# Performance work log

Measured on AMD Instinct MI355X. Metric: run time of the kernel, lower is better.

Reference implementation:

```python
import jax, jax.numpy as jnp
import numpy as np

B, T, C, H, N = 2, 2048, 2048, 32, 64
EPS_GN = 1e-5 * 8 ** 2  # eps * head_size_divisor^2


def _bf16(t):
    # kernel inputs are cast to bfloat16 in the original module
    return t.astype(jnp.bfloat16).astype(jnp.float32)


def _rwkv7_scan(r, k, v, w, a, b, s0):
    """Generalized delta-rule recurrence (fused_recurrent_rwkv7 semantics).
    r,k,v,w,a,b: [B,T,H,N]; s0: [B,H,N,N] with layout [key, value].
    S_t = diag(exp(w_t)) S + b_t (a_t^T S) + k_t v_t^T ; o_t = r_t^T S_t."""
    def step(S, ts):
        rt, kt, vt, wt, at, bt = ts  # each [B,H,N]
        sa = jnp.einsum('bhk,bhkv->bhv', at, S)
        S = S * jnp.exp(wt)[..., None] + bt[..., None] * sa[..., None, :] + kt[..., None] * vt[..., None, :]
        o = jnp.einsum('bhk,bhkv->bhv', rt, S)
        return S, o
    mv = lambda t: jnp.moveaxis(t, 1, 0)  # [B,T,H,N] -> [T,B,H,N]
    S, o = jax.lax.scan(step, s0, (mv(r), mv(k), mv(v), mv(w), mv(a), mv(b)))
    return jnp.moveaxis(o, 0, 1), S


def _forward(x, shift_state, wkv_state, v_first, x_r, x_w, x_k, x_v, x_a, x_g,
             w0, w1, w2, a0, a1, a2, v0, v1, v2, g1, g2, k_k, k_a, r_k,
             W_r, W_k, W_v, W_o, ln_w, ln_b):
    xx = jnp.concatenate([shift_state[:, None, :], x[:, :-1]], axis=1) - x
    xr, xw, xk, xv, xa, xg = (x + xx * m for m in (x_r, x_w, x_k, x_v, x_a, x_g))
    r = xr @ W_r
    w = -jax.nn.softplus(-(w0 + jnp.tanh(xw @ w1) @ w2)) - 0.5
    k = xk @ W_k
    v = xv @ W_v
    v = v + (v_first - v) * jax.nn.sigmoid(v0 + (xv @ v1) @ v2)  # layer_id > 0 branch
    a = jax.nn.sigmoid(a0 + (xa @ a1) @ a2)
    g = jax.nn.sigmoid(xg @ g1) @ g2
    kk = (k * k_k).reshape(B, T, H, N)
    kk = kk / jnp.maximum(jnp.linalg.norm(kk, axis=-1, keepdims=True), 1e-12)
    kk = kk.reshape(B, T, C)
    k = k * (1.0 + (a - 1.0) * k_a)
    hd = lambda t: _bf16(t).reshape(B, T, H, N)
    o, S = _rwkv7_scan(hd(r), hd(k), hd(v), hd(w), hd(-kk), hd(kk * a), wkv_state)
    y = o.reshape(B, T, H, N)
    # GroupNorm with H groups over C channels
    mu = y.mean(-1, keepdims=True)
    var = ((y - mu) ** 2).mean(-1, keepdims=True)
    y = ((y - mu) / jnp.sqrt(var + EPS_GN)).reshape(B, T, C) * ln_w + ln_b
    rr, k4, vv = r.reshape(B, T, H, N), k.reshape(B, T, H, N), v.reshape(B, T, H, N)
    y = y + ((rr * k4 * r_k).sum(-1, keepdims=True) * vv).reshape(B, T, C)
    out = (y * g) @ W_o
    return out, x[:, -1], S


def setup_inputs() -> dict:
    key = jax.random.key(0)
    ks = iter(jax.random.split(key, 40))
    rn = lambda shape, s=0.02: jax.random.normal(next(ks), shape, jnp.float32) * s
    ru = lambda shape: jax.random.uniform(next(ks), shape, jnp.float32)
    return dict(
        x=rn((B, T, C), 1.0), shift_state=rn((B, C), 1.0),
        wkv_state=jnp.zeros((B, H, N, N), jnp.float32), v_first=rn((B, T, C), 1.0),
        x_r=ru((1, 1, C)), x_w=ru((1, 1, C)), x_k=ru((1, 1, C)),
        x_v=ru((1, 1, C)), x_a=ru((1, 1, C)), x_g=ru((1, 1, C)),
        w0=rn((1, 1, C), 0.5) - 4.0, w1=rn((C, 64)), w2=rn((64, C)),
        a0=jnp.zeros((1, 1, C), jnp.float32), a1=rn((C, 64)), a2=rn((64, C)),
        v0=jnp.ones((1, 1, C), jnp.float32), v1=rn((C, 32)), v2=rn((32, C)),
        g1=rn((C, 128)), g2=rn((128, C)),
        k_k=jnp.full((1, 1, C), 0.85, jnp.float32), k_a=jnp.ones((1, 1, C), jnp.float32),
        r_k=rn((H, N), 0.1),
        W_r=rn((C, C), C ** -0.5), W_k=rn((C, C), C ** -0.5),
        W_v=rn((C, C), C ** -0.5), W_o=rn((C, C), C ** -0.5),
        ln_w=jnp.ones((C,), jnp.float32), ln_b=jnp.zeros((C,), jnp.float32))


def reference(x, shift_state, wkv_state, v_first, x_r, x_w, x_k, x_v, x_a, x_g,
              w0, w1, w2, a0, a1, a2, v0, v1, v2, g1, g2, k_k, k_a, r_k,
              W_r, W_k, W_v, W_o, ln_w, ln_b):
    return _forward(x, shift_state, wkv_state, v_first, x_r, x_w, x_k, x_v, x_a, x_g,
                    w0, w1, w2, a0, a1, a2, v0, v1, v2, g1, g2, k_k, k_a, r_k,
                    W_r, W_k, W_v, W_o, ln_w, ln_b)
```

## Files before the change

### kernel.cpp

```cpp
#include <hip/hip_runtime.h>
#include <cstdint>
#include <cmath>

#define B_ 2
#define T_ 2048
#define C_ 2048
#define H_ 32
#define BT_ (B_ * T_)
#define BTC_ ((size_t)B_ * T_ * C_)
#define L_ 128
#define NC_ 16

typedef __attribute__((ext_vector_type(4))) float f32x4;
typedef __attribute__((ext_vector_type(2))) float f32x2;
typedef __attribute__((ext_vector_type(8))) short bf16x8;
typedef __attribute__((ext_vector_type(4))) unsigned short us4;
typedef __attribute__((ext_vector_type(4))) int i32x4;

__device__ __forceinline__ unsigned short f2bf(float f) {
  union { float f; unsigned int u; } c; c.f = f;
  unsigned int u = c.u;
  return (unsigned short)((u + 0x7FFFu + ((u >> 16) & 1u)) >> 16);
}
__device__ __forceinline__ float bf2f(unsigned short h) {
  union { unsigned int u; float f; } c; c.u = ((unsigned int)h) << 16;
  return c.f;
}
__device__ __forceinline__ float rlane(float v, int lane) {
  return __int_as_float(__builtin_amdgcn_readlane(__float_as_int(v), lane));
}
__device__ __forceinline__ void split4(f32x4 v, us4& h, us4& l) {
  h.x = f2bf(v.x); l.x = f2bf(v.x - bf2f(h.x));
  h.y = f2bf(v.y); l.y = f2bf(v.y - bf2f(h.y));
  h.z = f2bf(v.z); l.z = f2bf(v.z - bf2f(h.z));
  h.w = f2bf(v.w); l.w = f2bf(v.w - bf2f(h.w));
}
__device__ __forceinline__ void g2l(const void* g, void* l) {
  __builtin_amdgcn_global_load_lds((const __attribute__((address_space(1))) void*)g,
                                   (__attribute__((address_space(3))) void*)l, 16, 0, 0);
}

__global__ __launch_bounds__(256) void k_mix(
    const float* __restrict__ x, const float* __restrict__ shift,
    const float* __restrict__ m_r, const float* __restrict__ m_w,
    const float* __restrict__ m_k, const float* __restrict__ m_v,
    const float* __restrict__ m_a, const float* __restrict__ m_g,
    unsigned short* __restrict__ r_h, unsigned short* __restrict__ r_l,
    unsigned short* __restrict__ k_h, unsigned short* __restrict__ k_l,
    unsigned short* __restrict__ v_h, unsigned short* __restrict__ v_l,
    unsigned short* __restrict__ o_w, unsigned short* __restrict__ o_a,
    unsigned short* __restrict__ o_g,
    float* __restrict__ xlast) {
  size_t i4 = ((size_t)blockIdx.x * 256 + threadIdx.x) * 4;
  int c = (int)(i4 % C_);
  size_t bt = i4 / C_;
  int t = (int)(bt % T_);
  int b = (int)(bt / T_);
  f32x4 xv = *(const f32x4*)(x + i4);
  f32x4 pv = (t == 0) ? *(const f32x4*)(shift + (size_t)b * C_ + c)
                      : *(const f32x4*)(x + i4 - C_);
  f32x4 dx = pv - xv;
#define MIXHL(mp, oh, ol) { f32x4 mm = *(const f32x4*)(mp + c); f32x4 rr = xv + dx * mm; \
    us4 hh, ll; split4(rr, hh, ll); *(us4*)(oh + i4) = hh; *(us4*)(ol + i4) = ll; }
#define MIXH(mp, oh) { f32x4 mm = *(const f32x4*)(mp + c); f32x4 rr = xv + dx * mm; \
    us4 pk; pk.x = f2bf(rr.x); pk.y = f2bf(rr.y); pk.z = f2bf(rr.z); pk.w = f2bf(rr.w); \
    *(us4*)(oh + i4) = pk; }
  MIXHL(m_r, r_h, r_l) MIXHL(m_k, k_h, k_l) MIXHL(m_v, v_h, v_l)
  MIXH(m_w, o_w) MIXH(m_a, o_a) MIXH(m_g, o_g)
#undef MIXHL
#undef MIXH
  if (t == T_ - 1) *(f32x4*)(xlast + (size_t)b * C_ + c) = xv;
}

__global__ __launch_bounds__(256) void k_tr(const float* __restrict__ in,
                                            unsigned short* __restrict__ out,
                                            int R, int Cc) {
  __shared__ float tile[32][33];
  int c0 = blockIdx.x * 32, r0 = blockIdx.y * 32;
  int tid = threadIdx.x;
  int rr = tid >> 3, c4 = (tid & 7) * 4;
  f32x4 v = *(const f32x4*)(in + (size_t)(r0 + rr) * Cc + c0 + c4);
  tile[rr][c4] = v.x; tile[rr][c4 + 1] = v.y; tile[rr][c4 + 2] = v.z; tile[rr][c4 + 3] = v.w;
  __syncthreads();
  int cc = tid >> 3, r4 = (tid & 7) * 4;
  us4 o;
  o.x = f2bf(tile[r4][cc]); o.y = f2bf(tile[r4 + 1][cc]);
  o.z = f2bf(tile[r4 + 2][cc]); o.w = f2bf(tile[r4 + 3][cc]);
  *(us4*)(out + (size_t)(c0 + cc) * R + r0 + r4) = o;
}

__global__ __launch_bounds__(256) void k_trs(const float* __restrict__ in,
                                             unsigned short* __restrict__ oh,
                                             unsigned short* __restrict__ ol,
                                             int R, int Cc) {
  __shared__ float tile[32][33];
  int c0 = blockIdx.x * 32, r0 = blockIdx.y * 32;
  int tid = threadIdx.x;
  int rr = tid >> 3, c4 = (tid & 7) * 4;
  f32x4 v = *(const f32x4*)(in + (size_t)(r0 + rr) * Cc + c0 + c4);
  tile[rr][c4] = v.x; tile[rr][c4 + 1] = v.y; tile[rr][c4 + 2] = v.z; tile[rr][c4 + 3] = v.w;
  __syncthreads();
  int cc = tid >> 3, r4 = (tid & 7) * 4;
  f32x4 w = { tile[r4][cc], tile[r4 + 1][cc], tile[r4 + 2][cc], tile[r4 + 3][cc] };
  us4 h, l; split4(w, h, l);
  size_t o = (size_t)(c0 + cc) * R + r0 + r4;
  *(us4*)(oh + o) = h; *(us4*)(ol + o) = l;
}

__global__ __launch_bounds__(256) void k_gemm(
    const unsigned short* __restrict__ X, const unsigned short* __restrict__ Wt,
    void* __restrict__ out, int M, int N, int K, int mode) {
  __shared__ alignas(16) unsigned short As[128 * 32];
  __shared__ alignas(16) unsigned short Bs[128 * 32];
  const int tid = threadIdx.x;
  const int lane = tid & 63, wave = tid >> 6;
  const int wr = wave >> 1, wc = wave & 1;
  const int lm = lane & 15, lq = lane >> 4;
  const int gx = gridDim.x;
  const int nwg = gx * gridDim.y;
  const int bid = blockIdx.y * gx + blockIdx.x;
  const int sz = (bid & 7) * (nwg >> 3) + (bid >> 3);
  const int m0 = (sz / gx) * 128, n0 = (sz % gx) * 128;
  const int srow = (lane >> 2);
  const int kcol = (lane & 3) * 8;
  f32x4 acc[4][4];
#pragma unroll
  for (int i = 0; i < 4; ++i)
#pragma unroll
    for (int j = 0; j < 4; ++j) acc[i][j] = (f32x4){0.f, 0.f, 0.f, 0.f};

  for (int k0 = 0; k0 < K; k0 += 32) {
#pragma unroll
    for (int p = 0; p < 2; ++p) {
      int row = wave * 32 + p * 16 + srow;
      g2l(X + (size_t)(m0 + row) * K + k0 + kcol, As + (wave * 2 + p) * 512);
      int n = n0 + row; if (n > N - 1) n = N - 1;
      g2l(Wt + (size_t)n * K + k0 + kcol, Bs + (wave * 2 + p) * 512);
    }
    __syncthreads();
    bf16x8 af[4], bfr[4];
#pragma unroll
    for (int i = 0; i < 4; ++i)
      af[i] = *(const bf16x8*)(As + (size_t)(wr * 64 + i * 16 + lm) * 32 + lq * 8);
#pragma unroll
    for (int j = 0; j < 4; ++j)
      bfr[j] = *(const bf16x8*)(Bs + (size_t)(wc * 64 + j * 16 + lm) * 32 + lq * 8);
#pragma unroll
    for (int i = 0; i < 4; ++i)
#pragma unroll
      for (int j = 0; j < 4; ++j)
        acc[i][j] = __builtin_amdgcn_mfma_f32_16x16x32_bf16(af[i], bfr[j], acc[i][j], 0, 0, 0);
    __syncthreads();
  }
#pragma unroll
  for (int i = 0; i < 4; ++i)
#pragma unroll
    for (int j = 0; j < 4; ++j) {
      int n = n0 + wc * 64 + j * 16 + lm;
      if (n >= N) continue;
      int mb = m0 + wr * 64 + i * 16 + lq * 4;
#pragma unroll
      for (int r = 0; r < 4; ++r) {
        float val = acc[i][j][r];
        size_t off = (size_t)(mb + r) * N + n;
        if (mode == 0) {
          ((float*)out)[off] = val;
        } else {
          if (mode == 2) val = tanhf(val);
          else if (mode == 3) val = 1.0f / (1.0f + __expf(-val));
          ((unsigned short*)out)[off] = f2bf(val);
        }
      }
    }
}

__global__ __launch_bounds__(256) void k_gemm2(
    const unsigned short* __restrict__ Xh, const unsigned short* __restrict__ Xl, int xlo,
    const unsigned short* __restrict__ Wh, const unsigned short* __restrict__ Wl, int wlo,
    void* __restrict__ out, int M, int N, int K, int mode) {
  __shared__ alignas(16) unsigned short Ah[128 * 32];
  __shared__ alignas(16) unsigned short Al[128 * 32];
  __shared__ alignas(16) unsigned short Bh[128 * 32];
  __shared__ alignas(16) unsigned short Bl[128 * 32];
  const int tid = threadIdx.x;
  const int lane = tid & 63, wave = tid >> 6;
  const int wr = wave >> 1, wc = wave & 1;
  const int lm = lane & 15, lq = lane >> 4;
  const int gx = gridDim.x;
  const int nwg = gx * gridDim.y;
  const int bid = blockIdx.y * gx + blockIdx.x;
  const int sz = (bid & 7) * (nwg >> 3) + (bid >> 3);
  const int m0 = (sz / gx) * 128, n0 = (sz % gx) * 128;
  const int srow = (lane >> 2);
  const int kcol = (lane & 3) * 8;
  f32x4 acc[4][4];
#pragma unroll
  for (int i = 0; i < 4; ++i)
#pragma unroll
    for (int j = 0; j < 4; ++j) acc[i][j] = (f32x4){0.f, 0.f, 0.f, 0.f};

  for (int k0 = 0; k0 < K; k0 += 32) {
#pragma unroll
    for (int p = 0; p < 2; ++p) {
      int row = wave * 32 + p * 16 + srow;
      int off = (wave * 2 + p) * 512;
      size_t ga = (size_t)(m0 + row) * K + k0 + kcol;
      g2l(Xh + ga, Ah + off);
      if (xlo) g2l(Xl + ga, Al + off);
      int n = n0 + row; if (n > N - 1) n = N - 1;
      size_t gb = (size_t)n * K + k0 + kcol;
      g2l(Wh + gb, Bh + off);
      if (wlo) g2l(Wl + gb, Bl + off);
    }
    __syncthreads();
    bf16x8 ah[4], bh[4];
#pragma unroll
    for (int i = 0; i < 4; ++i)
      ah[i] = *(const bf16x8*)(Ah + (size_t)(wr * 64 + i * 16 + lm) * 32 + lq * 8);
#pragma unroll
    for (int j = 0; j < 4; ++j)
      bh[j] = *(const bf16x8*)(Bh + (size_t)(wc * 64 + j * 16 + lm) * 32 + lq * 8);
#pragma unroll
    for (int i = 0; i < 4; ++i)
#pragma unroll
      for (int j = 0; j < 4; ++j)
        acc[i][j] = __builtin_amdgcn_mfma_f32_16x16x32_bf16(ah[i], bh[j], acc[i][j], 0, 0, 0);
    if (xlo) {
      bf16x8 al[4];
#pragma unroll
      for (int i = 0; i < 4; ++i)
        al[i] = *(const bf16x8*)(Al + (size_t)(wr * 64 + i * 16 + lm) * 32 + lq * 8);
#pragma unroll
      for (int i = 0; i < 4; ++i)
#pragma unroll
        for (int j = 0; j < 4; ++j)
          acc[i][j] = __builtin_amdgcn_mfma_f32_16x16x32_bf16(al[i], bh[j], acc[i][j], 0, 0, 0);
    }
    if (wlo) {
      bf16x8 bl[4];
#pragma unroll
      for (int j = 0; j < 4; ++j)
        bl[j] = *(const bf16x8*)(Bl + (size_t)(wc * 64 + j * 16 + lm) * 32 + lq * 8);
#pragma unroll
      for (int i = 0; i < 4; ++i)
#pragma unroll
        for (int j = 0; j < 4; ++j)
          acc[i][j] = __builtin_amdgcn_mfma_f32_16x16x32_bf16(ah[i], bl[j], acc[i][j], 0, 0, 0);
    }
    __syncthreads();
  }
#pragma unroll
  for (int i = 0; i < 4; ++i)
#pragma unroll
    for (int j = 0; j < 4; ++j) {
      int n = n0 + wc * 64 + j * 16 + lm;
      if (n >= N) continue;
      int mb = m0 + wr * 64 + i * 16 + lq * 4;
#pragma unroll
      for (int r = 0; r < 4; ++r) {
        float val = acc[i][j][r];
        size_t off = (size_t)(mb + r) * N + n;
        if (mode == 0) {
          ((float*)out)[off] = val;
        } else {
          if (mode == 2) val = tanhf(val);
          else if (mode == 3) val = 1.0f / (1.0f + __expf(-val));
          ((unsigned short*)out)[off] = f2bf(val);
        }
      }
    }
}

__global__ __launch_bounds__(256) void k_pre(
    const float* __restrict__ rp, const float* __restrict__ kp, float* __restrict__ vp,
    const unsigned short* __restrict__ ww, const unsigned short* __restrict__ aa,
    const unsigned short* __restrict__ vv,
    const float* __restrict__ vfirst,
    const float* __restrict__ w0, const float* __restrict__ a0, const float* __restrict__ v0,
    const float* __restrict__ kkc, const float* __restrict__ kac,
    const float* __restrict__ rkw,
    unsigned short* __restrict__ rb, unsigned short* __restrict__ wb,
    unsigned short* __restrict__ kb, unsigned short* __restrict__ vb,
    unsigned short* __restrict__ ab, unsigned short* __restrict__ bb,
    float* __restrict__ dp) {
  int gw = blockIdx.x * 4 + (threadIdx.x >> 6);
  int l = threadIdx.x & 63;
  int h = gw & (H_ - 1);
  size_t bt = (size_t)(gw >> 5);
  size_t idx = bt * C_ + h * 64 + l;
  int c = h * 64 + l;
  float rf = rp[idx], kf = kp[idx], vr = vp[idx];
  float z = -(w0[c] + bf2f(ww[idx]));
  float sp = (z > 15.f) ? z : log1pf(__expf(z));
  float wv = -sp - 0.5f;
  float ag = 1.f / (1.f + __expf(-(a0[c] + bf2f(aa[idx]))));
  float sv = 1.f / (1.f + __expf(-(v0[c] + bf2f(vv[idx]))));
  float vf = vr + (vfirst[idx] - vr) * sv;
  float kkv = kf * kkc[c];
  float ss = kkv * kkv;
#pragma unroll
  for (int m = 1; m < 64; m <<= 1) ss += __shfl_xor(ss, m);
  float nrm = fmaxf(sqrtf(ss), 1e-12f);
  float kkn = kkv / nrm;
  float ks = kf * (1.f + (ag - 1.f) * kac[c]);
  vp[idx] = vf;
  float bon = rf * ks * rkw[c];
#pragma unroll
  for (int m = 1; m < 64; m <<= 1) bon += __shfl_xor(bon, m);
  if (l == 0) dp[bt * H_ + h] = bon;
  rb[idx] = f2bf(rf); wb[idx] = f2bf(wv); kb[idx] = f2bf(ks);
  vb[idx] = f2bf(vf); ab[idx] = f2bf(-kkn); bb[idx] = f2bf(kkn * ag);
}

__global__ __launch_bounds__(256) void k_scanP(
    const unsigned short* __restrict__ rb,
    const unsigned short* __restrict__ wb, const unsigned short* __restrict__ kb,
    const unsigned short* __restrict__ vb, const unsigned short* __restrict__ ab,
    const unsigned short* __restrict__ bb,
    float* __restrict__ Pg, float* __restrict__ Ug,
    unsigned short* __restrict__ Zg, float* __restrict__ o) {
  const int blk = blockIdx.x;
  const int c = blk & (NC_ - 1), bh = blk >> 4;
  const int b = bh >> 5, h = bh & (H_ - 1);
  const int l = threadIdx.x & 63;
  const int kg = __builtin_amdgcn_readfirstlane(threadIdx.x >> 6);
  const int kg16 = kg * 16;
  __shared__ f32x4 part[2][256];
  size_t base = (size_t)b * ((size_t)T_ * C_) + (size_t)(c * L_) * C_ + h * 64 + l;
  size_t zbase = (size_t)blk * 8192;
  float P[16], U[16];
#pragma unroll
  for (int i = 0; i < 16; ++i) { P[i] = (kg16 + i == l) ? 1.f : 0.f; U[i] = 0.f; }
  float pr[4], pw[4], pk[4], pv[4], pa[4], pb[4];
#pragma unroll
  for (int s = 0; s < 4; ++s) {
    size_t a_ = base + (size_t)s * C_;
    pr[s] = bf2f(rb[a_]);
    pw[s] = bf2f(wb[a_]); pk[s] = bf2f(kb[a_]); pv[s] = bf2f(vb[a_]);
    pa[s] = bf2f(ab[a_]); pb[s] = bf2f(bb[a_]);
  }
  float saP = pa[0];
  float saU = 0.f;
  for (int t0 = 0; t0 < L_; t0 += 4) {
#pragma unroll
    for (int u = 0; u < 4; ++u) {
      const int t = t0 + u;
      float rl_ = pr[u], wl = pw[u], kl = pk[u], vl = pv[u], bl = pb[u];
      float an = pa[(u + 1) & 3];
      if (t + 4 < L_) {
        size_t a_ = base + (size_t)(t + 4) * C_;
        pr[u] = bf2f(rb[a_]);
        pw[u] = bf2f(wb[a_]); pk[u] = bf2f(kb[a_]); pv[u] = bf2f(vb[a_]);
        pa[u] = bf2f(ab[a_]); pb[u] = bf2f(bb[a_]);
      }
      float ew = exp2f(wl * 1.4426950408889634f);
      float psP = 0.f, psU = 0.f, zs = 0.f, ys = 0.f;
#pragma unroll
      for (int i = 0; i < 16; ++i) {
        int ki = kg16 + i;
        float ewk = rlane(ew, ki), bk = rlane(bl, ki), kk = rlane(kl, ki);
        P[i] = fmaf(P[i], ewk, bk * saP);
        U[i] = fmaf(U[i], ewk, fmaf(bk, saU, kk * vl));
        float ak = rlane(an, ki), rk = rlane(rl_, ki);
        psP = fmaf(ak, P[i], psP);
        psU = fmaf(ak, U[i], psU);
        zs = fmaf(rk, P[i], zs);
        ys = fmaf(rk, U[i], ys);
      }
      part[t & 1][kg * 64 + l] = (f32x4){psP, psU, zs, ys};
      __syncthreads();
      f32x4 q0 = part[t & 1][l], q1 = part[t & 1][64 + l],
            q2 = part[t & 1][128 + l], q3 = part[t & 1][192 + l];
      saP = (q0.x + q1.x) + (q2.x + q3.x);
      saU = (q0.y + q1.y) + (q2.y + q3.y);
      if (kg == 0) {
        o[base + (size_t)t * C_] = (q0.w + q1.w) + (q2.w + q3.w);
      } else if (kg == 1) {
        Zg[zbase + t * 64 + l] = f2bf((q0.z + q1.z) + (q2.z + q3.z));
      }
    }
  }
  size_t pb_ = (size_t)blk * 4096;
#pragma unroll
  for (int i = 0; i < 16; ++i) {
    Pg[pb_ + (size_t)l * 64 + kg16 + i] = P[i];
    Ug[pb_ + (size_t)(kg16 + i) * 64 + l] = U[i];
  }
}

__global__ __launch_bounds__(256) void k_scanC(
    const float* __restrict__ Pg, const float* __restrict__ Ug,
    const float* __restrict__ s0, float* __restrict__ Scg, float* __restrict__ sout) {
  const int bh = blockIdx.x;
  const int l = threadIdx.x & 63;
  const int kg = __builtin_amdgcn_readfirstlane(threadIdx.x >> 6);
  const int kg16 = kg * 16;
  const int tid = threadIdx.x;
  __shared__ float Sb[4096];
#pragma unroll
  for (int q = 0; q < 4; ++q) {
    int e = tid * 16 + q * 4;
    *(f32x4*)(Sb + e) = *(const f32x4*)(s0 + (size_t)bh * 4096 + e);
  }
  __syncthreads();
  for (int c = 0; c < NC_; ++c) {
    size_t cb = ((size_t)bh * NC_ + c) * 4096;
#pragma unroll
    for (int q = 0; q < 4; ++q) {
      int e = tid * 16 + q * 4;
      *(f32x4*)(Scg + cb + e) = *(const f32x4*)(Sb + e);
    }
    const float* Pt = Pg + cb;
    const float* Uc = Ug + cb;
    float acc[16];
#pragma unroll
    for (int i = 0; i < 16; ++i) acc[i] = Uc[(size_t)(kg16 + i) * 64 + l];
    for (int j = 0; j < 64; ++j) {
      float s = Sb[j * 64 + l];
#pragma unroll
      for (int i = 0; i < 16; ++i) acc[i] = fmaf(Pt[j * 64 + kg16 + i], s, acc[i]);
    }
    __syncthreads();
#pragma unroll
    for (int i = 0; i < 16; ++i) Sb[(kg16 + i) * 64 + l] = acc[i];
    __syncthreads();
  }
#pragma unroll
  for (int q = 0; q < 4; ++q) {
    int e = tid * 16 + q * 4;
    *(f32x4*)(sout + (size_t)bh * 4096 + e) = *(const f32x4*)(Sb + e);
  }
}

__global__ __launch_bounds__(256) void k_scanO(
    const unsigned short* __restrict__ Zg, const float* __restrict__ Scg,
    float* __restrict__ o) {
  const int blk = blockIdx.x;
  const int c = blk & (NC_ - 1), bh = blk >> 4;
  const int b = bh >> 5, h = bh & (H_ - 1);
  const int l = threadIdx.x & 63;
  const int w = threadIdx.x >> 6;
  float S[64];
  const float* Sp = Scg + (size_t)blk * 4096 + l;
#pragma unroll
  for (int k = 0; k < 64; ++k) S[k] = Sp[(size_t)k * 64];
  size_t zb = (size_t)blk * 8192;
  size_t ob = (size_t)b * ((size_t)T_ * C_) + (size_t)(c * L_) * C_ + h * 64 + l;
  for (int tt = 0; tt < 32; ++tt) {
    int t = w * 32 + tt;
    float zv = bf2f(Zg[zb + t * 64 + l]);
    float a0_ = 0.f, a1_ = 0.f, a2_ = 0.f, a3_ = 0.f;
#pragma unroll
    for (int k = 0; k < 64; k += 4) {
      a0_ = fmaf(rlane(zv, k), S[k], a0_);
      a1_ = fmaf(rlane(zv, k + 1), S[k + 1], a1_);
      a2_ = fmaf(rlane(zv, k + 2), S[k + 2], a2_);
      a3_ = fmaf(rlane(zv, k + 3), S[k + 3], a3_);
    }
    o[ob + (size_t)t * C_] += (a0_ + a1_) + (a2_ + a3_);
  }
}

__global__ __launch_bounds__(256) void k_post(
    const float* __restrict__ o, const float* __restrict__ vp, const float* __restrict__ gp,
    const float* __restrict__ dp,
    const float* __restrict__ lnw, const float* __restrict__ lnb,
    unsigned short* __restrict__ z) {
  int gw = blockIdx.x * 4 + (threadIdx.x >> 6);
  int l = threadIdx.x & 63;
  int h = gw & (H_ - 1);
  size_t bt = (size_t)(gw >> 5);
  size_t idx = bt * C_ + h * 64 + l;
  int c = h * 64 + l;
  float ov = o[idx];
  float s1 = ov;
#pragma unroll
  for (int m = 1; m < 64; m <<= 1) s1 += __shfl_xor(s1, m);
  float mu = s1 * (1.f / 64.f);
  float d = ov - mu;
  float s2 = d * d;
#pragma unroll
  for (int m = 1; m < 64; m <<= 1) s2 += __shfl_xor(s2, m);
  float var = s2 * (1.f / 64.f);
  float y = d * rsqrtf(var + 6.4e-4f);
  y = y * lnw[c] + lnb[c];
  y = fmaf(dp[bt * H_ + h], vp[idx], y);
  z[idx] = f2bf(y * gp[idx]);
}

extern "C" void kernel_launch(void* const* d_in, const int* in_sizes, int n_in,
                              void* d_out, int out_size, void* d_ws, size_t ws_size,
                              hipStream_t stream) {
  const float* x      = (const float*)d_in[0];
  const float* shift  = (const float*)d_in[1];
  const float* wkv    = (const float*)d_in[2];
  const float* vfirst = (const float*)d_in[3];
  const float* x_r    = (const float*)d_in[4];
  const float* x_w    = (const float*)d_in[5];
  const float* x_k    = (const float*)d_in[6];
  const float* x_v    = (const float*)d_in[7];
  const float* x_a    = (const float*)d_in[8];
  const float* x_g    = (const float*)d_in[9];
  const float* w0     = (const float*)d_in[10];
  const float* w1     = (const float*)d_in[11];
  const float* w2     = (const float*)d_in[12];
  const float* a0     = (const float*)d_in[13];
  const float* a1     = (const float*)d_in[14];
  const float* a2     = (const float*)d_in[15];
  const float* v0     = (const float*)d_in[16];
  const float* v1     = (const float*)d_in[17];
  const float* v2     = (const float*)d_in[18];
  const float* g1     = (const float*)d_in[19];
  const float* g2     = (const float*)d_in[20];
  const float* k_k    = (const float*)d_in[21];
  const float* k_a    = (const float*)d_in[22];
  const float* r_k    = (const float*)d_in[23];
  const float* W_r    = (const float*)d_in[24];
  const float* W_k    = (const float*)d_in[25];
  const float* W_v    = (const float*)d_in[26];
  const float* W_o    = (const float*)d_in[27];
  const float* ln_w   = (const float*)d_in[28];
  const float* ln_b   = (const float*)d_in[29];

  char* wp = (char*)d_ws;
  auto alloc = [&](size_t bytes) { char* p = wp; wp += (bytes + 255) & ~(size_t)255; return p; };
  const size_t SB = BTC_ * 2;
  const size_t SF = BTC_ * 4;

  unsigned short* w1t = (unsigned short*)alloc((size_t)C_ * 64 * 2);
  unsigned short* w2t = (unsigned short*)alloc((size_t)C_ * 64 * 2);
  unsigned short* a1t = (unsigned short*)alloc((size_t)C_ * 64 * 2);
  unsigned short* a2t = (unsigned short*)alloc((size_t)C_ * 64 * 2);
  unsigned short* v1t = (unsigned short*)alloc((size_t)C_ * 32 * 2);
  unsigned short* v2t = (unsigned short*)alloc((size_t)C_ * 32 * 2);
  unsigned short* g1t = (unsigned short*)alloc((size_t)C_ * 128 * 2);
  unsigned short* g2t = (unsigned short*)alloc((size_t)C_ * 128 * 2);
  unsigned short* hw  = (unsigned short*)alloc((size_t)BT_ * 64 * 2);
  unsigned short* ha  = (unsigned short*)alloc((size_t)BT_ * 64 * 2);
  unsigned short* hv  = (unsigned short*)alloc((size_t)BT_ * 32 * 2);
  unsigned short* hg  = (unsigned short*)alloc((size_t)BT_ * 128 * 2);
  unsigned short* Wt2 = (unsigned short*)alloc((size_t)C_ * C_ * 2 * 2);
  float* dp           = (float*)alloc((size_t)BT_ * H_ * 4);
  unsigned short* xw  = (unsigned short*)alloc(SB);
  unsigned short* xa  = (unsigned short*)alloc(SB);
  unsigned short* xg  = (unsigned short*)alloc(SB);
  unsigned short* xr2 = (unsigned short*)alloc(2 * SB);
  unsigned short* xk2 = (unsigned short*)alloc(2 * SB);
  unsigned short* xv2 = (unsigned short*)alloc(2 * SB);
  float* rbuf         = (float*)alloc(SF);
  unsigned short* vbb = (unsigned short*)alloc(SB);

  unsigned short* Wh = Wt2;
  unsigned short* Wl = Wt2 + (size_t)C_ * C_;
  unsigned short* xr_h = xr2, *xr_l = xr2 + BTC_;
  unsigned short* xk_h = xk2, *xk_l = xk2 + BTC_;
  unsigned short* xv_h = xv2, *xv_l = xv2 + BTC_;
  float* kbuf = (float*)xr2;
  float* vbuf = (float*)xk2;
  unsigned short* rb = xv2;
  unsigned short* kb = xv2 + BTC_;
  float* gfull = rbuf;
  unsigned short* zbuf = (unsigned short*)xr2;
  float* Pg  = (float*)xr2;
  float* Ug  = Pg + (size_t)1024 * 4096;
  unsigned short* zg = Wt2;
  float* Scg = (float*)xw;

  float* outp  = (float*)d_out;
  float* xlast = outp + BTC_;
  float* soutp = outp + BTC_ + (size_t)B_ * C_;
  float* obuf  = outp;

  auto tr = [&](const float* in, unsigned short* out, int R, int Cc) {
    k_tr<<<dim3(Cc / 32, R / 32), 256, 0, stream>>>(in, out, R, Cc);
  };
  auto gemm = [&](const unsigned short* X, const unsigned short* Wtp, void* out,
                  int M, int N, int K, int mode) {
    k_gemm<<<dim3((N + 127) / 128, M / 128), 256, 0, stream>>>(X, Wtp, out, M, N, K, mode);
  };
  auto gemm2 = [&](const unsigned short* Xh_, const unsigned short* Xl_, int xlo,
                   const unsigned short* Wh_, const unsigned short* Wl_, int wlo,
                   void* out, int M, int N, int K, int mode) {
    k_gemm2<<<dim3((N + 127) / 128, M / 128), 256, 0, stream>>>(Xh_, Xl_, xlo, Wh_, Wl_, wlo,
                                                                out, M, N, K, mode);
  };

  k_mix<<<(int)(BTC_ / 4 / 256), 256, 0, stream>>>(x, shift, x_r, x_w, x_k, x_v, x_a, x_g,
                                                   xr_h, xr_l, xk_h, xk_l, xv_h, xv_l,
                                                   xw, xa, xg, xlast);
  tr(w1, w1t, C_, 64);  tr(w2, w2t, 64, C_);
  tr(a1, a1t, C_, 64);  tr(a2, a2t, 64, C_);
  tr(v1, v1t, C_, 32);  tr(v2, v2t, 32, C_);
  tr(g1, g1t, C_, 128); tr(g2, g2t, 128, C_);

  gemm(xw, w1t, hw, BT_, 64, C_, 2);
  gemm(xa, a1t, ha, BT_, 64, C_, 1);
  gemm2(xv_h, xv_l, 1, v1t, nullptr, 0, hv, BT_, 32, C_, 1);
  gemm(xg, g1t, hg, BT_, 128, C_, 3);

  k_trs<<<dim3(C_ / 32, C_ / 32), 256, 0, stream>>>(W_r, Wh, Wl, C_, C_);
  gemm2(xr_h, xr_l, 1, Wh, Wl, 1, rbuf, BT_, C_, C_, 0);
  k_trs<<<dim3(C_ / 32, C_ / 32), 256, 0, stream>>>(W_k, Wh, Wl, C_, C_);
  gemm2(xk_h, xk_l, 1, Wh, Wl, 1, kbuf, BT_, C_, C_, 0);
  k_trs<<<dim3(C_ / 32, C_ / 32), 256, 0, stream>>>(W_v, Wh, Wl, C_, C_);
  gemm2(xv_h, xv_l, 1, Wh, Wl, 1, vbuf, BT_, C_, C_, 0);

  gemm(hw, w2t, xw, BT_, C_, 64, 1);
  gemm(ha, a2t, xa, BT_, C_, 64, 1);
  gemm(hv, v2t, xg, BT_, C_, 32, 1);

  k_pre<<<BT_ * H_ / 4, 256, 0, stream>>>(rbuf, kbuf, vbuf, xw, xa, xg, vfirst,
                                          w0, a0, v0, k_k, k_a, r_k,
                                          rb, xw, kb, vbb, xa, xg, dp);

  gemm(hg, g2t, gfull, BT_, C_, 128, 0);

  k_scanP<<<B_ * H_ * NC_, 256, 0, stream>>>(rb, xw, kb, vbb, xa, xg, Pg, Ug, zg, obuf);
  k_scanC<<<B_ * H_, 256, 0, stream>>>(Pg, Ug, wkv, Scg, soutp);
  k_scanO<<<B_ * H_ * NC_, 256, 0, stream>>>(zg, Scg, obuf);

  k_post<<<BT_ * H_ / 4, 256, 0, stream>>>(obuf, vbuf, gfull, dp, ln_w, ln_b, zbuf);

  tr(W_o, Wh, C_, C_);
  gemm(zbuf, Wh, outp, BT_, C_, C_, 0);
}
```

Before: 1.466 ms.

## Split rank-1 delta update to shorten scan critical path across barrier

The chunked scan kernel now applies the decay and k·v update first and computes the partial reductions against the decayed state. The b·sa correction is added algebraically afterward using wave-wide dot products (a·b, r·b) obtained through xor shuffles. The reduction of the previous step is read after the next step's independent work, so LDS latency overlaps compute and only one barrier remains per step. It adds two shuffle reductions and a second pass over P/U per step, and it changes the floating-point summation order.

After: 1.662 ms. 13.3% more time.

```diff
diff --git a/kernel.cpp b/kernel.cpp
--- a/kernel.cpp
+++ b/kernel.cpp
@@ -331,53 +331,76 @@
   float P[16], U[16];
 #pragma unroll
   for (int i = 0; i < 16; ++i) { P[i] = (kg16 + i == l) ? 1.f : 0.f; U[i] = 0.f; }
-  float pr[4], pw[4], pk[4], pv[4], pa[4], pb[4];
+  float pr[4], pw[4], pk[4], pv[4], pb[4], pa[4];
 #pragma unroll
   for (int s = 0; s < 4; ++s) {
     size_t a_ = base + (size_t)s * C_;
-    pr[s] = bf2f(rb[a_]);
-    pw[s] = bf2f(wb[a_]); pk[s] = bf2f(kb[a_]); pv[s] = bf2f(vb[a_]);
-    pa[s] = bf2f(ab[a_]); pb[s] = bf2f(bb[a_]);
-  }
-  float saP = pa[0];
-  float saU = 0.f;
+    pr[s] = bf2f(rb[a_]); pw[s] = bf2f(wb[a_]); pk[s] = bf2f(kb[a_]);
+    pv[s] = bf2f(vb[a_]); pb[s] = bf2f(bb[a_]);
+    pa[s] = bf2f(ab[base + (size_t)(s + 1) * C_]);
+  }
+  float a0l = bf2f(ab[base]);
+  float saP = 0.f, saU = 0.f;
+  float cP = 0.f, cU = 0.f, cZ = 0.f, cY = 0.f;
   for (int t0 = 0; t0 < L_; t0 += 4) {
 #pragma unroll
     for (int u = 0; u < 4; ++u) {
       const int t = t0 + u;
-      float rl_ = pr[u], wl = pw[u], kl = pk[u], vl = pv[u], bl = pb[u];
-      float an = pa[(u + 1) & 3];
+      float rl_ = pr[u], wl = pw[u], kl = pk[u], vl = pv[u], bl = pb[u], al = pa[u];
       if (t + 4 < L_) {
         size_t a_ = base + (size_t)(t + 4) * C_;
-        pr[u] = bf2f(rb[a_]);
-        pw[u] = bf2f(wb[a_]); pk[u] = bf2f(kb[a_]); pv[u] = bf2f(vb[a_]);
-        pa[u] = bf2f(ab[a_]); pb[u] = bf2f(bb[a_]);
+        pr[u] = bf2f(rb[a_]); pw[u] = bf2f(wb[a_]); pk[u] = bf2f(kb[a_]);
+        pv[u] = bf2f(vb[a_]); pb[u] = bf2f(bb[a_]);
+        int ta = t + 5; if (ta > L_ - 1) ta = L_ - 1;
+        pa[u] = bf2f(ab[base + (size_t)ta * C_]);
       }
       float ew = exp2f(wl * 1.4426950408889634f);
-      float psP = 0.f, psU = 0.f, zs = 0.f, ys = 0.f;
+      float dab = al * bl, drb = rl_ * bl;
+#pragma unroll
+      for (int m = 1; m < 64; m <<= 1) { dab += __shfl_xor(dab, m); drb += __shfl_xor(drb, m); }
+      float pP = 0.f, pU = 0.f, zP = 0.f, yU = 0.f;
 #pragma unroll
       for (int i = 0; i < 16; ++i) {
         int ki = kg16 + i;
-        float ewk = rlane(ew, ki), bk = rlane(bl, ki), kk = rlane(kl, ki);
-        P[i] = fmaf(P[i], ewk, bk * saP);
-        U[i] = fmaf(U[i], ewk, fmaf(bk, saU, kk * vl));
-        float ak = rlane(an, ki), rk = rlane(rl_, ki);
-        psP = fmaf(ak, P[i], psP);
-        psU = fmaf(ak, U[i], psU);
-        zs = fmaf(rk, P[i], zs);
-        ys = fmaf(rk, U[i], ys);
+        float ewk = rlane(ew, ki), kk = rlane(kl, ki);
+        float Pp = P[i] * ewk;
+        float Up = fmaf(U[i], ewk, kk * vl);
+        P[i] = Pp; U[i] = Up;
+        float ak = rlane(al, ki), rk = rlane(rl_, ki);
+        pP = fmaf(ak, Pp, pP); zP = fmaf(rk, Pp, zP);
+        pU = fmaf(ak, Up, pU); yU = fmaf(rk, Up, yU);
       }
-      part[t & 1][kg * 64 + l] = (f32x4){psP, psU, zs, ys};
+      if (t > 0) {
+        f32x4 q0 = part[t & 1][l], q1 = part[t & 1][64 + l],
+              q2 = part[t & 1][128 + l], q3 = part[t & 1][192 + l];
+        saP = ((q0.x + q1.x) + (q2.x + q3.x)) + cP;
+        saU = ((q0.y + q1.y) + (q2.y + q3.y)) + cU;
+        if (kg == 0) {
+          o[base + (size_t)(t - 1) * C_] = ((q0.w + q1.w) + (q2.w + q3.w)) + cY;
+        } else if (kg == 1) {
+          Zg[zbase + (t - 1) * 64 + l] = f2bf(((q0.z + q1.z) + (q2.z + q3.z)) + cZ);
+        }
+      } else {
+        saP = a0l; saU = 0.f;
+      }
+#pragma unroll
+      for (int i = 0; i < 16; ++i) {
+        float bk = rlane(bl, kg16 + i);
+        P[i] = fmaf(bk, saP, P[i]);
+        U[i] = fmaf(bk, saU, U[i]);
+      }
+      cP = saP * dab; cU = saU * dab; cZ = saP * drb; cY = saU * drb;
+      part[(t + 1) & 1][kg * 64 + l] = (f32x4){pP, pU, zP, yU};
       __syncthreads();
-      f32x4 q0 = part[t & 1][l], q1 = part[t & 1][64 + l],
-            q2 = part[t & 1][128 + l], q3 = part[t & 1][192 + l];
-      saP = (q0.x + q1.x) + (q2.x + q3.x);
-      saU = (q0.y + q1.y) + (q2.y + q3.y);
-      if (kg == 0) {
-        o[base + (size_t)t * C_] = (q0.w + q1.w) + (q2.w + q3.w);
-      } else if (kg == 1) {
-        Zg[zbase + t * 64 + l] = f2bf((q0.z + q1.z) + (q2.z + q3.z));
-      }
+    }
+  }
+  {
+    f32x4 q0 = part[0][l], q1 = part[0][64 + l],
+          q2 = part[0][128 + l], q3 = part[0][192 + l];
+    if (kg == 0) {
+      o[base + (size_t)(L_ - 1) * C_] = ((q0.w + q1.w) + (q2.w + q3.w)) + cY;
+    } else if (kg == 1) {
+      Zg[zbase + (L_ - 1) * 64 + l] = f2bf(((q0.z + q1.z) + (q2.z + q3.z)) + cZ);
     }
   }
   size_t pb_ = (size_t)blk * 4096;
```

## Run chunk-scan with one wavefront per block, removing LDS reductions and barriers

Applied to the files above, without the earlier changes.

The chunked scan kernel now uses a single 64-lane wavefront per (batch, head, chunk) that holds all 64 state rows in registers, in place of four waves each holding 16 rows. This drops the per-timestep shared-memory partial-sum exchange and __syncthreads, and the reductions are split across four independent accumulators. The 'a' vector is now prefetched one step ahead and the final P store is vectorised. In exchange, per-thread register pressure rises sharply (128 state floats), blocks shrink to 64 threads, and each wave does four times the serial FMA work per step, so latency hiding may get worse.

Measured after the change: 1.408 ms. 1.04x faster.

```diff
diff --git a/kernel.cpp b/kernel.cpp
--- a/kernel.cpp
+++ b/kernel.cpp
@@ -312,7 +312,7 @@
   vb[idx] = f2bf(vf); ab[idx] = f2bf(-kkn); bb[idx] = f2bf(kkn * ag);
 }
 
-__global__ __launch_bounds__(256) void k_scanP(
+__global__ __launch_bounds__(64) void k_scanP(
     const unsigned short* __restrict__ rb,
     const unsigned short* __restrict__ wb, const unsigned short* __restrict__ kb,
     const unsigned short* __restrict__ vb, const unsigned short* __restrict__ ab,
@@ -323,69 +323,70 @@
   const int c = blk & (NC_ - 1), bh = blk >> 4;
   const int b = bh >> 5, h = bh & (H_ - 1);
   const int l = threadIdx.x & 63;
-  const int kg = __builtin_amdgcn_readfirstlane(threadIdx.x >> 6);
-  const int kg16 = kg * 16;
-  __shared__ f32x4 part[2][256];
   size_t base = (size_t)b * ((size_t)T_ * C_) + (size_t)(c * L_) * C_ + h * 64 + l;
   size_t zbase = (size_t)blk * 8192;
-  float P[16], U[16];
-#pragma unroll
-  for (int i = 0; i < 16; ++i) { P[i] = (kg16 + i == l) ? 1.f : 0.f; U[i] = 0.f; }
-  float pr[4], pw[4], pk[4], pv[4], pa[4], pb[4];
+  float P[64], U[64];
+#pragma unroll
+  for (int k = 0; k < 64; ++k) { P[k] = (k == l) ? 1.f : 0.f; U[k] = 0.f; }
+  float pr[4], pw[4], pk[4], pv[4], pb[4], pa[4];
 #pragma unroll
   for (int s = 0; s < 4; ++s) {
     size_t a_ = base + (size_t)s * C_;
-    pr[s] = bf2f(rb[a_]);
-    pw[s] = bf2f(wb[a_]); pk[s] = bf2f(kb[a_]); pv[s] = bf2f(vb[a_]);
-    pa[s] = bf2f(ab[a_]); pb[s] = bf2f(bb[a_]);
-  }
-  float saP = pa[0];
-  float saU = 0.f;
+    pr[s] = bf2f(rb[a_]); pw[s] = bf2f(wb[a_]); pk[s] = bf2f(kb[a_]);
+    pv[s] = bf2f(vb[a_]); pb[s] = bf2f(bb[a_]);
+    pa[s] = bf2f(ab[base + (size_t)(s + 1) * C_]);
+  }
+  float saP = bf2f(ab[base]), saU = 0.f;
   for (int t0 = 0; t0 < L_; t0 += 4) {
 #pragma unroll
     for (int u = 0; u < 4; ++u) {
       const int t = t0 + u;
-      float rl_ = pr[u], wl = pw[u], kl = pk[u], vl = pv[u], bl = pb[u];
-      float an = pa[(u + 1) & 3];
+      float rl_ = pr[u], wl = pw[u], kl = pk[u], vl = pv[u], bl = pb[u], al = pa[u];
       if (t + 4 < L_) {
         size_t a_ = base + (size_t)(t + 4) * C_;
-        pr[u] = bf2f(rb[a_]);
-        pw[u] = bf2f(wb[a_]); pk[u] = bf2f(kb[a_]); pv[u] = bf2f(vb[a_]);
-        pa[u] = bf2f(ab[a_]); pb[u] = bf2f(bb[a_]);
+        pr[u] = bf2f(rb[a_]); pw[u] = bf2f(wb[a_]); pk[u] = bf2f(kb[a_]);
+        pv[u] = bf2f(vb[a_]); pb[u] = bf2f(bb[a_]);
+        int ta = t + 5; if (ta > L_ - 1) ta = L_ - 1;
+        pa[u] = bf2f(ab[base + (size_t)ta * C_]);
       }
       float ew = exp2f(wl * 1.4426950408889634f);
-      float psP = 0.f, psU = 0.f, zs = 0.f, ys = 0.f;
-#pragma unroll
-      for (int i = 0; i < 16; ++i) {
-        int ki = kg16 + i;
-        float ewk = rlane(ew, ki), bk = rlane(bl, ki), kk = rlane(kl, ki);
-        P[i] = fmaf(P[i], ewk, bk * saP);
-        U[i] = fmaf(U[i], ewk, fmaf(bk, saU, kk * vl));
-        float ak = rlane(an, ki), rk = rlane(rl_, ki);
-        psP = fmaf(ak, P[i], psP);
-        psU = fmaf(ak, U[i], psU);
-        zs = fmaf(rk, P[i], zs);
-        ys = fmaf(rk, U[i], ys);
+      float zz0 = 0.f, zz1 = 0.f, zz2 = 0.f, zz3 = 0.f;
+      float yy0 = 0.f, yy1 = 0.f, yy2 = 0.f, yy3 = 0.f;
+      float qp0 = 0.f, qp1 = 0.f, qp2 = 0.f, qp3 = 0.f;
+      float qu0 = 0.f, qu1 = 0.f, qu2 = 0.f, qu3 = 0.f;
+#pragma unroll
+      for (int k = 0; k < 64; k += 4) {
+#define STEPK(kk, ZZ, YY, QP, QU)                                        \
+        {                                                                \
+          float s_ew = rlane(ew, kk), s_b = rlane(bl, kk),               \
+                s_k = rlane(kl, kk);                                     \
+          float Pn = fmaf(P[kk], s_ew, s_b * saP);                       \
+          float Un = fmaf(U[kk], s_ew, fmaf(s_b, saU, s_k * vl));        \
+          P[kk] = Pn; U[kk] = Un;                                        \
+          float s_r = rlane(rl_, kk), s_a = rlane(al, kk);               \
+          ZZ = fmaf(s_r, Pn, ZZ); YY = fmaf(s_r, Un, YY);                \
+          QP = fmaf(s_a, Pn, QP); QU = fmaf(s_a, Un, QU);                \
+        }
+        STEPK(k,     zz0, yy0, qp0, qu0)
+        STEPK(k + 1, zz1, yy1, qp1, qu1)
+        STEPK(k + 2, zz2, yy2, qp2, qu2)
+        STEPK(k + 3, zz3, yy3, qp3, qu3)
+#undef STEPK
       }
-      part[t & 1][kg * 64 + l] = (f32x4){psP, psU, zs, ys};
-      __syncthreads();
-      f32x4 q0 = part[t & 1][l], q1 = part[t & 1][64 + l],
-            q2 = part[t & 1][128 + l], q3 = part[t & 1][192 + l];
-      saP = (q0.x + q1.x) + (q2.x + q3.x);
-      saU = (q0.y + q1.y) + (q2.y + q3.y);
-      if (kg == 0) {
-        o[base + (size_t)t * C_] = (q0.w + q1.w) + (q2.w + q3.w);
-      } else if (kg == 1) {
-        Zg[zbase + t * 64 + l] = f2bf((q0.z + q1.z) + (q2.z + q3.z));
-      }
+      o[base + (size_t)t * C_] = (yy0 + yy1) + (yy2 + yy3);
+      Zg[zbase + t * 64 + l] = f2bf((zz0 + zz1) + (zz2 + zz3));
+      saP = (qp0 + qp1) + (qp2 + qp3);
+      saU = (qu0 + qu1) + (qu2 + qu3);
     }
   }
   size_t pb_ = (size_t)blk * 4096;
 #pragma unroll
-  for (int i = 0; i < 16; ++i) {
-    Pg[pb_ + (size_t)l * 64 + kg16 + i] = P[i];
-    Ug[pb_ + (size_t)(kg16 + i) * 64 + l] = U[i];
-  }
+  for (int k4 = 0; k4 < 64; k4 += 4) {
+    f32x4 pv4 = { P[k4], P[k4 + 1], P[k4 + 2], P[k4 + 3] };
+    *(f32x4*)(Pg + pb_ + (size_t)l * 64 + k4) = pv4;
+  }
+#pragma unroll
+  for (int k = 0; k < 64; ++k) Ug[pb_ + (size_t)k * 64 + l] = U[k];
 }
 
 __global__ __launch_bounds__(256) void k_scanC(
@@ -615,7 +616,7 @@
 
   gemm(hg, g2t, gfull, BT_, C_, 128, 0);
 
-  k_scanP<<<B_ * H_ * NC_, 256, 0, stream>>>(rb, xw, kb, vbb, xa, xg, Pg, Ug, zg, obuf);
+  k_scanP<<<B_ * H_ * NC_, 64, 0, stream>>>(rb, xw, kb, vbb, xa, xg, Pg, Ug, zg, obuf);
   k_scanC<<<B_ * H_, 256, 0, stream>>>(Pg, Ug, wkv, Scg, soutp);
   k_scanO<<<B_ * H_ * NC_, 256, 0, stream>>>(zg, Scg, obuf);
 
```
